# Optimization experiments

Measured on AMD Instinct MI355X. Metric: run time of the kernel, lower is better.

## Reference

```python
import jax, jax.numpy as jnp
import numpy as np

N1, F_IN, E1 = 50000, 128, 1000000   # data1: 10 graphs x 5000 nodes
B, NPG = 10, 5000
N2, E2 = 199, 4000                    # data2: fixed by fc1 in-dim 9950 = 50*199
K = 50
LN_EPS = 1e-5


def setup_inputs() -> dict:
    key = jax.random.key(0)
    ks = jax.random.split(key, 24)
    s = lambda k, shape: (jax.random.normal(k, shape, jnp.float32) * 0.05)
    inp = {}
    inp["x1"] = jax.random.normal(ks[0], (N1, F_IN), jnp.float32)
    inp["edge_index1"] = jax.random.randint(ks[1], (2, E1), 0, N1, jnp.int32)
    inp["batch1"] = jnp.repeat(jnp.arange(B, dtype=jnp.int32), NPG)  # equal-size graphs
    inp["x2"] = jax.random.normal(ks[2], (N2, F_IN), jnp.float32)
    inp["edge_index2"] = jax.random.randint(ks[3], (2, E2), 0, N2, jnp.int32)
    # GNN params (shared Siamese weights). PyG SAGEConv: lin_l (aggr, has bias), lin_r (root, no bias)
    inp["w1l"] = s(ks[4], (128, F_IN)); inp["b1l"] = jnp.zeros((128,), jnp.float32)
    inp["w1r"] = s(ks[5], (128, F_IN))
    inp["w2l"] = s(ks[6], (64, 128));   inp["b2l"] = jnp.zeros((64,), jnp.float32)
    inp["w2r"] = s(ks[7], (64, 128))
    # MLP head
    inp["fc1_w"] = s(ks[8], (128, K * N2)); inp["fc1_b"] = jnp.zeros((128,), jnp.float32)
    inp["ln1_g"] = jnp.ones((128,), jnp.float32); inp["ln1_b"] = jnp.zeros((128,), jnp.float32)
    inp["fc2_w"] = s(ks[9], (64, 128)); inp["fc2_b"] = jnp.zeros((64,), jnp.float32)
    inp["ln2_g"] = jnp.ones((64,), jnp.float32); inp["ln2_b"] = jnp.zeros((64,), jnp.float32)
    inp["fc3_w"] = s(ks[10], (1, 64)); inp["fc3_b"] = jnp.zeros((1,), jnp.float32)
    return inp


def _sage(x, edge_index, wl, bl, wr, n_nodes):
    # mean aggregation of source features at target nodes, then two linears
    src, dst = edge_index[0], edge_index[1]
    msg_sum = jax.ops.segment_sum(x[src], dst, num_segments=n_nodes)
    cnt = jax.ops.segment_sum(jnp.ones((edge_index.shape[1], 1), x.dtype), dst,
                              num_segments=n_nodes)
    mean = msg_sum / jnp.maximum(cnt, 1.0)
    return mean @ wl.T + bl + x @ wr.T


def _gnn(x, ei, w1l, b1l, w1r, w2l, b2l, w2r):
    n = x.shape[0]
    h = jax.nn.relu(_sage(x, ei, w1l, b1l, w1r, n))
    return jax.nn.relu(_sage(h, ei, w2l, b2l, w2r, n))


def _layernorm(x, g, b):
    mu = jnp.mean(x, -1, keepdims=True)
    var = jnp.mean((x - mu) ** 2, -1, keepdims=True)
    return (x - mu) * jax.lax.rsqrt(var + LN_EPS) * g + b


def reference(x1, edge_index1, batch1, x2, edge_index2,
              w1l, b1l, w1r, w2l, b2l, w2r,
              fc1_w, fc1_b, ln1_g, ln1_b, fc2_w, fc2_b, ln2_g, ln2_b, fc3_w, fc3_b):
    out1 = _gnn(x1, edge_index1, w1l, b1l, w1r, w2l, b2l, w2r)   # [N1, 64]
    out2 = _gnn(x2, edge_index2, w1l, b1l, w1r, w2l, b2l, w2r)   # [N2, 64]
    # cdist p=2
    a2 = jnp.sum(out1 * out1, -1, keepdims=True)                 # [N1,1]
    b2 = jnp.sum(out2 * out2, -1)                                # [N2]
    d2 = a2 + b2[None, :] - 2.0 * (out1 @ out2.T)
    dist = jnp.sqrt(jnp.maximum(d2, 0.0))                        # [N1, N2]
    # SortAggregation(k=50): per-graph sort rows by last column (desc), take top k.
    # batch1 groups equal-size graphs contiguously -> reshape is exact dense batching.
    xb = dist.reshape(B, NPG, N2)
    order = jnp.argsort(-xb[:, :, -1], axis=1)[:, :K]            # [B, K]
    topk = jnp.take_along_axis(xb, order[:, :, None], axis=1)    # [B, K, N2]
    out = topk.reshape(B, K * N2)
    out = jax.nn.relu(_layernorm(out @ fc1_w.T + fc1_b, ln1_g, ln1_b))
    out = jax.nn.relu(_layernorm(out @ fc2_w.T + fc2_b, ln2_g, ln2_b))
    out = jax.nn.sigmoid(out @ fc3_w.T + fc3_b)                  # [B, 1]
    return out
```

## Files before the change

### kernel.cpp

```cpp
#include <hip/hip_runtime.h>
#include <math.h>

#define N1 50000
#define F_IN 128
#define E1 1000000
#define Bg 10
#define NPG 5000
#define N2 199
#define E2 4000
#define KSEL 50
#define LN_EPS 1e-5f
#define CHUNKS 16
#define CHSZ 313
#define EBT 4096
#define NB 196
#define BCAP 6144

typedef unsigned long long ull;

__global__ void k_bucket(const int* __restrict__ ei1, int* __restrict__ bcnt,
                         unsigned int* __restrict__ bed,
                         const int* __restrict__ ei2, int* __restrict__ rp2,
                         int* __restrict__ srcs2) {
  int t = threadIdx.x;
  int blk = blockIdx.x;
  const int nEdgeBlocks = (E1 + EBT - 1) / EBT;
  if (blk == nEdgeBlocks) {
    __shared__ int cnt2[N2];
    __shared__ int cur2[N2];
    const int* src = ei2;
    const int* dst = ei2 + E2;
    for (int i = t; i < N2; i += 256) cnt2[i] = 0;
    __syncthreads();
    for (int e = t; e < E2; e += 256) atomicAdd(&cnt2[dst[e]], 1);
    __syncthreads();
    if (t == 0) {
      int run = 0;
      rp2[0] = 0;
      for (int i = 0; i < N2; i++) {
        cur2[i] = run;
        run += cnt2[i];
        rp2[i + 1] = run;
      }
    }
    __syncthreads();
    for (int e = t; e < E2; e += 256) {
      int d = dst[e];
      int pos = atomicAdd(&cur2[d], 1);
      srcs2[pos] = src[e];
    }
    return;
  }
  __shared__ int hcnt[NB];
  const int* src = ei1;
  const int* dst = ei1 + E1;
  int e0 = blk * EBT;
  int e1 = min(e0 + EBT, E1);
  if (t < NB) hcnt[t] = 0;
  __syncthreads();
  for (int e = e0 + t; e < e1; e += 256) atomicAdd(&hcnt[dst[e] >> 8], 1);
  __syncthreads();
  if (t < NB) hcnt[t] = atomicAdd(&bcnt[t], hcnt[t]);
  __syncthreads();
  for (int e = e0 + t; e < e1; e += 256) {
    int d = dst[e];
    int s = src[e];
    int b = d >> 8;
    int pos = atomicAdd(&hcnt[b], 1);
    if (pos < BCAP)
      bed[(size_t)b * BCAP + pos] = ((unsigned int)(d & 255) << 16) | (unsigned int)s;
  }
}

__global__ __launch_bounds__(1024) void k_csr_bucket(
    const int* __restrict__ bcnt, const unsigned int* __restrict__ bed,
    int* __restrict__ rp, int* __restrict__ srcs) {
  __shared__ int cnt[256];
  __shared__ int cur[256];
  __shared__ int wsums[4];
  __shared__ int s_bbase;
  int b = blockIdx.x, t = threadIdx.x;
  int lane = t & 63, w = t >> 6;
  int total = min(bcnt[b], BCAP);
  if (t < 256) cnt[t] = 0;
  if (w == 0) {
    int vb = 0;
    for (int i = lane; i < b; i += 64) vb += min(bcnt[i], BCAP);
    for (int off = 32; off; off >>= 1) vb += __shfl_xor(vb, off);
    if (lane == 0) s_bbase = vb;
  }
  __syncthreads();
  const unsigned int* list = bed + (size_t)b * BCAP;
  for (int e = t; e < total; e += 1024) atomicAdd(&cnt[list[e] >> 16], 1);
  __syncthreads();
  int incl = 0, v = 0;
  if (t < 256) {
    v = cnt[t];
    int x = v;
#pragma unroll
    for (int off = 1; off < 64; off <<= 1) {
      int y = __shfl_up(x, off);
      if (lane >= off) x += y;
    }
    if (lane == 63) wsums[w] = x;
    incl = x;
  }
  __syncthreads();
  if (t < 256) {
    int pre = 0;
    for (int i = 0; i < w; i++) pre += wsums[i];
    incl += pre;
    int bbase = s_bbase;
    int node = b * 256 + t;
    if (node < N1) rp[node + 1] = bbase + incl;
    cur[t] = bbase + incl - v;
    if (b == 0 && t == 0) rp[0] = 0;
  }
  __syncthreads();
  for (int e = t; e < total; e += 1024) {
    unsigned int pe = list[e];
    int pos = atomicAdd(&cur[pe >> 16], 1);
    srcs[pos] = (int)(pe & 0xFFFFu);
  }
}

__global__ void k_aggr128(const float* __restrict__ xA, const int* __restrict__ rpA,
                          const int* __restrict__ srcsA, float* __restrict__ meanA, int nA,
                          const float* __restrict__ xB, const int* __restrict__ rpB,
                          const int* __restrict__ srcsB, float* __restrict__ meanB, int nB,
                          int blocksA) {
  int blk = blockIdx.x;
  const float* x;
  const int* rp;
  const int* srcs;
  float* mean;
  int n, nb0;
  if (blk < blocksA) { x = xA; rp = rpA; srcs = srcsA; mean = meanA; n = nA; nb0 = blk * 4; }
  else { x = xB; rp = rpB; srcs = srcsB; mean = meanB; n = nB; nb0 = (blk - blocksA) * 4; }
  int lane = threadIdx.x & 63;
  int node = nb0 + (threadIdx.x >> 6);
  if (node >= n) return;
  int s = rp[node], e = rp[node + 1];
  int half = lane >> 5;
  int sub = lane & 31;
  const float4* xp = (const float4*)x;
  float4 acc = make_float4(0.f, 0.f, 0.f, 0.f);
  int i = s;
  for (; i + 8 <= e; i += 8) {
    int s0 = srcs[i + half];
    int s1 = srcs[i + 2 + half];
    int s2 = srcs[i + 4 + half];
    int s3 = srcs[i + 6 + half];
    float4 v0 = xp[(size_t)s0 * 32 + sub];
    float4 v1 = xp[(size_t)s1 * 32 + sub];
    float4 v2 = xp[(size_t)s2 * 32 + sub];
    float4 v3 = xp[(size_t)s3 * 32 + sub];
    acc.x += (v0.x + v1.x) + (v2.x + v3.x);
    acc.y += (v0.y + v1.y) + (v2.y + v3.y);
    acc.z += (v0.z + v1.z) + (v2.z + v3.z);
    acc.w += (v0.w + v1.w) + (v2.w + v3.w);
  }
  for (; i + 2 <= e; i += 2) {
    int s0 = srcs[i + half];
    float4 v = xp[(size_t)s0 * 32 + sub];
    acc.x += v.x; acc.y += v.y; acc.z += v.z; acc.w += v.w;
  }
  if (i < e && half == 0) {
    float4 v = xp[(size_t)srcs[i] * 32 + sub];
    acc.x += v.x; acc.y += v.y; acc.z += v.z; acc.w += v.w;
  }
  acc.x += __shfl_xor(acc.x, 32);
  acc.y += __shfl_xor(acc.y, 32);
  acc.z += __shfl_xor(acc.z, 32);
  acc.w += __shfl_xor(acc.w, 32);
  if (half == 0) {
    float c = (float)((e - s) > 0 ? (e - s) : 1);
    float inv = 1.f / c;
    float4 o = make_float4(acc.x * inv, acc.y * inv, acc.z * inv, acc.w * inv);
    ((float4*)mean)[(size_t)node * 32 + sub] = o;
  }
}

__global__ void k_aggr_fused64(const float* __restrict__ zA, const int* __restrict__ rpA,
                               const int* __restrict__ srcsA, float* __restrict__ outA, int nA,
                               const float* __restrict__ zB, const int* __restrict__ rpB,
                               const int* __restrict__ srcsB, float* __restrict__ outB, int nB,
                               const float* __restrict__ bias, int blocksA) {
  int blk = blockIdx.x;
  const float* zlr;
  const int* rp;
  const int* srcs;
  float* out;
  int n, nb0;
  if (blk < blocksA) { zlr = zA; rp = rpA; srcs = srcsA; out = outA; n = nA; nb0 = blk * 4; }
  else { zlr = zB; rp = rpB; srcs = srcsB; out = outB; n = nB; nb0 = (blk - blocksA) * 4; }
  int lane = threadIdx.x & 63;
  int node = nb0 + (threadIdx.x >> 6);
  if (node >= n) return;
  int s = rp[node], e = rp[node + 1];
  int q = lane >> 4;
  int sub = lane & 15;
  const float4* zp = (const float4*)zlr;
  float4 acc = make_float4(0.f, 0.f, 0.f, 0.f);
  int i = s;
  for (; i + 8 <= e; i += 8) {
    int s0 = srcs[i + q];
    int s1 = srcs[i + 4 + q];
    float4 v0 = zp[(size_t)s0 * 32 + sub];
    float4 v1 = zp[(size_t)s1 * 32 + sub];
    acc.x += v0.x + v1.x;
    acc.y += v0.y + v1.y;
    acc.z += v0.z + v1.z;
    acc.w += v0.w + v1.w;
  }
  for (; i + 4 <= e; i += 4) {
    int s0 = srcs[i + q];
    float4 v = zp[(size_t)s0 * 32 + sub];
    acc.x += v.x; acc.y += v.y; acc.z += v.z; acc.w += v.w;
  }
  int rem = e - i;
  if (q < rem) {
    int s0 = srcs[i + q];
    float4 v = zp[(size_t)s0 * 32 + sub];
    acc.x += v.x; acc.y += v.y; acc.z += v.z; acc.w += v.w;
  }
  acc.x += __shfl_xor(acc.x, 16);
  acc.y += __shfl_xor(acc.y, 16);
  acc.z += __shfl_xor(acc.z, 16);
  acc.w += __shfl_xor(acc.w, 16);
  acc.x += __shfl_xor(acc.x, 32);
  acc.y += __shfl_xor(acc.y, 32);
  acc.z += __shfl_xor(acc.z, 32);
  acc.w += __shfl_xor(acc.w, 32);
  if (q == 0) {
    float c = (float)((e - s) > 0 ? (e - s) : 1);
    float inv = 1.f / c;
    float4 mb = ((const float4*)bias)[sub];
    float4 rt = zp[(size_t)node * 32 + 16 + sub];
    float v0 = acc.x * inv + mb.x + rt.x;
    float v1 = acc.y * inv + mb.y + rt.y;
    float v2 = acc.z * inv + mb.z + rt.z;
    float v3 = acc.w * inv + mb.w + rt.w;
    float4 o;
    o.x = v0 > 0.f ? v0 : 0.f;
    o.y = v1 > 0.f ? v1 : 0.f;
    o.z = v2 > 0.f ? v2 : 0.f;
    o.w = v3 > 0.f ? v3 : 0.f;
    ((float4*)out)[(size_t)node * 16 + sub] = o;
  }
}

__global__ __launch_bounds__(256) void k_sage_gemm128(
    const float* __restrict__ xinA, const float* __restrict__ meanA,
    float* __restrict__ outA, int nA,
    const float* __restrict__ xinB, const float* __restrict__ meanB,
    float* __restrict__ outB, int nB,
    const float* __restrict__ wl, const float* __restrict__ bl,
    const float* __restrict__ wr, int blocksA) {
  constexpr int TM = 128, TK = 32;
  constexpr int SA = TM + 4;
  constexpr int SW = 128 + 4;
  __shared__ float s_a[TK][SA];
  __shared__ float s_w[TK][SW];
  int blk = blockIdx.x;
  const float* xin;
  const float* mean;
  float* out;
  int n, m0;
  if (blk < blocksA) { xin = xinA; mean = meanA; out = outA; n = nA; m0 = blk * TM; }
  else { xin = xinB; mean = meanB; out = outB; n = nB; m0 = (blk - blocksA) * TM; }
  int t = threadIdx.x;
  int tx = t & 15, ty = t >> 4;
  int sub = t >> 3;
  int kv = (t & 7) << 2;

  float acc[8][8];
#pragma unroll
  for (int i = 0; i < 8; i++)
#pragma unroll
    for (int j = 0; j < 8; j++) acc[i][j] = 0.f;

  for (int ph = 0; ph < 2; ph++) {
    const float* A = ph ? xin : mean;
    const float* W = ph ? wr : wl;
    for (int k0 = 0; k0 < 128; k0 += TK) {
      __syncthreads();
#pragma unroll
      for (int p = 0; p < 4; p++) {
        int node = m0 + p * 32 + sub;
        float4 v = make_float4(0.f, 0.f, 0.f, 0.f);
        if (node < n) v = *(const float4*)&A[(size_t)node * 128 + k0 + kv];
        int col = p * 32 + sub;
        s_a[kv + 0][col] = v.x;
        s_a[kv + 1][col] = v.y;
        s_a[kv + 2][col] = v.z;
        s_a[kv + 3][col] = v.w;
      }
#pragma unroll
      for (int p = 0; p < 4; p++) {
        int j = p * 32 + sub;
        float4 v = *(const float4*)&W[(size_t)j * 128 + k0 + kv];
        s_w[kv + 0][j] = v.x;
        s_w[kv + 1][j] = v.y;
        s_w[kv + 2][j] = v.z;
        s_w[kv + 3][j] = v.w;
      }
      __syncthreads();
#pragma unroll 8
      for (int kk = 0; kk < TK; kk++) {
        float4 a0 = *(const float4*)&s_a[kk][ty * 8];
        float4 a1 = *(const float4*)&s_a[kk][ty * 8 + 4];
        float av[8] = {a0.x, a0.y, a0.z, a0.w, a1.x, a1.y, a1.z, a1.w};
        float4 w0 = *(const float4*)&s_w[kk][tx * 8];
        float4 w1 = *(const float4*)&s_w[kk][tx * 8 + 4];
        float wv[8] = {w0.x, w0.y, w0.z, w0.w, w1.x, w1.y, w1.z, w1.w};
#pragma unroll
        for (int i = 0; i < 8; i++)
#pragma unroll
          for (int j = 0; j < 8; j++) acc[i][j] = fmaf(av[i], wv[j], acc[i][j]);
      }
    }
  }
  float bj[8];
#pragma unroll
  for (int j = 0; j < 8; j++) bj[j] = bl[tx * 8 + j];
#pragma unroll
  for (int i = 0; i < 8; i++) {
    int node = m0 + ty * 8 + i;
    if (node < n) {
#pragma unroll
      for (int q = 0; q < 8; q += 4) {
        float v0 = acc[i][q + 0] + bj[q + 0];
        float v1 = acc[i][q + 1] + bj[q + 1];
        float v2 = acc[i][q + 2] + bj[q + 2];
        float v3 = acc[i][q + 3] + bj[q + 3];
        float4 o;
        o.x = v0 > 0.f ? v0 : 0.f;
        o.y = v1 > 0.f ? v1 : 0.f;
        o.z = v2 > 0.f ? v2 : 0.f;
        o.w = v3 > 0.f ? v3 : 0.f;
        *(float4*)&out[(size_t)node * 128 + tx * 8 + q] = o;
      }
    }
  }
}

__global__ __launch_bounds__(256) void k_lin_dual(
    const float* __restrict__ AA, float* __restrict__ zA, int nA,
    const float* __restrict__ AB, float* __restrict__ zB, int nB,
    const float* __restrict__ wl, const float* __restrict__ wr, int blocksA) {
  constexpr int TM = 128, TK = 32;
  constexpr int SA = TM + 4;
  constexpr int SW = 128 + 4;
  __shared__ float s_a[TK][SA];
  __shared__ float s_w[TK][SW];
  int blk = blockIdx.x;
  const float* A;
  float* zlr;
  int n, m0;
  if (blk < blocksA) { A = AA; zlr = zA; n = nA; m0 = blk * TM; }
  else { A = AB; zlr = zB; n = nB; m0 = (blk - blocksA) * TM; }
  int t = threadIdx.x;
  int tx = t & 15, ty = t >> 4;
  int sub = t >> 3;
  int kv = (t & 7) << 2;

  float acc[8][8];
#pragma unroll
  for (int i = 0; i < 8; i++)
#pragma unroll
    for (int j = 0; j < 8; j++) acc[i][j] = 0.f;

  for (int k0 = 0; k0 < 128; k0 += TK) {
    __syncthreads();
#pragma unroll
    for (int p = 0; p < 4; p++) {
      int node = m0 + p * 32 + sub;
      float4 v = make_float4(0.f, 0.f, 0.f, 0.f);
      if (node < n) v = *(const float4*)&A[(size_t)node * 128 + k0 + kv];
      int col = p * 32 + sub;
      s_a[kv + 0][col] = v.x;
      s_a[kv + 1][col] = v.y;
      s_a[kv + 2][col] = v.z;
      s_a[kv + 3][col] = v.w;
    }
#pragma unroll
    for (int p = 0; p < 4; p++) {
      int j = p * 32 + sub;
      const float* W = (j < 64) ? &wl[(size_t)j * 128] : &wr[(size_t)(j - 64) * 128];
      float4 v = *(const float4*)&W[k0 + kv];
      s_w[kv + 0][j] = v.x;
      s_w[kv + 1][j] = v.y;
      s_w[kv + 2][j] = v.z;
      s_w[kv + 3][j] = v.w;
    }
    __syncthreads();
#pragma unroll 8
    for (int kk = 0; kk < TK; kk++) {
      float4 a0 = *(const float4*)&s_a[kk][ty * 8];
      float4 a1 = *(const float4*)&s_a[kk][ty * 8 + 4];
      float av[8] = {a0.x, a0.y, a0.z, a0.w, a1.x, a1.y, a1.z, a1.w};
      float4 w0 = *(const float4*)&s_w[kk][tx * 8];
      float4 w1 = *(const float4*)&s_w[kk][tx * 8 + 4];
      float wv[8] = {w0.x, w0.y, w0.z, w0.w, w1.x, w1.y, w1.z, w1.w};
#pragma unroll
      for (int i = 0; i < 8; i++)
#pragma unroll
        for (int j = 0; j < 8; j++) acc[i][j] = fmaf(av[i], wv[j], acc[i][j]);
    }
  }
#pragma unroll
  for (int i = 0; i < 8; i++) {
    int node = m0 + ty * 8 + i;
    if (node < n) {
#pragma unroll
      for (int q = 0; q < 8; q += 4) {
        float4 o = make_float4(acc[i][q + 0], acc[i][q + 1], acc[i][q + 2], acc[i][q + 3]);
        *(float4*)&zlr[(size_t)node * 128 + tx * 8 + q] = o;
      }
    }
  }
}

__global__ void k_score_topk_local(const float* __restrict__ out1,
                                   const float* __restrict__ out2,
                                   ull* __restrict__ cand) {
  __shared__ ull s[512];
  __shared__ float brow[64];
  int blk = blockIdx.x;
  int b = blk >> 4, c = blk & 15;
  int t = threadIdx.x;
  if (t < 64) brow[t] = out2[198 * 64 + t];
  __syncthreads();
  const float4* b4 = (const float4*)brow;
  float b2 = 0.f;
#pragma unroll
  for (int q = 0; q < 16; q++) {
    float4 w = b4[q];
    b2 = fmaf(w.x, w.x, fmaf(w.y, w.y, fmaf(w.z, w.z, fmaf(w.w, w.w, b2))));
  }
#pragma unroll
  for (int p = 0; p < 2; p++) {
    int i = p * 256 + t;
    ull key = 0ULL;
    int gidx = c * CHSZ + i;
    if (i < CHSZ && gidx < NPG) {
      const float4* ap = (const float4*)&out1[((size_t)b * NPG + gidx) * 64];
      float dot = 0.f, a2 = 0.f;
#pragma unroll
      for (int q = 0; q < 16; q++) {
        float4 a = ap[q];
        float4 w = b4[q];
        dot = fmaf(a.x, w.x, fmaf(a.y, w.y, fmaf(a.z, w.z, fmaf(a.w, w.w, dot))));
        a2 = fmaf(a.x, a.x, fmaf(a.y, a.y, fmaf(a.z, a.z, fmaf(a.w, a.w, a2))));
      }
      float d2 = a2 + b2 - 2.f * dot;
      float sc = sqrtf(fmaxf(d2, 0.f));
      key = ((ull)__float_as_uint(sc) << 32) | (unsigned int)(~gidx);
    }
    s[i] = key;
  }
  __syncthreads();
  for (int k = 2; k <= 512; k <<= 1) {
    for (int j = k >> 1; j > 0; j >>= 1) {
#pragma unroll
      for (int p = 0; p < 2; p++) {
        int i = p * 256 + t;
        int l = i ^ j;
        if (l > i) {
          bool up = ((i & k) != 0);
          ull a = s[i], bb = s[l];
          if ((a > bb) == up) { s[i] = bb; s[l] = a; }
        }
      }
      __syncthreads();
    }
  }
  if (t < KSEL) cand[(b * CHUNKS + c) * KSEL + t] = s[t];
}

__global__ void k_topk_merge(const ull* __restrict__ cand, int* __restrict__ sel) {
  __shared__ ull s[1024];
  int b = blockIdx.x, t = threadIdx.x;
#pragma unroll
  for (int p = 0; p < 4; p++) {
    int i = p * 256 + t;
    s[i] = (i < CHUNKS * KSEL) ? cand[b * CHUNKS * KSEL + i] : 0ULL;
  }
  __syncthreads();
  for (int k = 2; k <= 1024; k <<= 1) {
    for (int j = k >> 1; j > 0; j >>= 1) {
#pragma unroll
      for (int p = 0; p < 4; p++) {
        int i = p * 256 + t;
        int l = i ^ j;
        if (l > i) {
          bool up = ((i & k) != 0);
          ull a = s[i], bb = s[l];
          if ((a > bb) == up) { s[i] = bb; s[l] = a; }
        }
      }
      __syncthreads();
    }
  }
  if (t < KSEL) {
    int gidx = (int)(~((unsigned int)s[t]));
    sel[b * KSEL + t] = b * NPG + gidx;
  }
}

__global__ void k_dist_rows(const float* __restrict__ out1, const float* __restrict__ out2,
                            const int* __restrict__ sel, float* __restrict__ D) {
  __shared__ float arow[64];
  int i = blockIdx.x;
  int t = threadIdx.x;
  int node = sel[i];
  if (t < 64) arow[t] = out1[(size_t)node * 64 + t];
  __syncthreads();
  float a2 = 0.f;
#pragma unroll
  for (int f = 0; f < 64; f++) a2 = fmaf(arow[f], arow[f], a2);
  for (int nn = t; nn < N2; nn += 256) {
    float dot = 0.f, b2 = 0.f;
#pragma unroll 8
    for (int f = 0; f < 64; f++) {
      float bv = out2[nn * 64 + f];
      dot = fmaf(arow[f], bv, dot);
      b2 = fmaf(bv, bv, b2);
    }
    float d2 = a2 + b2 - 2.f * dot;
    D[i * N2 + nn] = sqrtf(fmaxf(d2, 0.f));
  }
}

__global__ void k_fc1_dot(const float* __restrict__ D, const float* __restrict__ w,
                          float* __restrict__ h1pre) {
  constexpr int M = KSEL * N2;
  constexpr int M2 = M / 2;
  int j = blockIdx.x;
  int t = threadIdx.x;
  const float2* wp = (const float2*)(w + (size_t)j * M);
  float acc[Bg];
#pragma unroll
  for (int b = 0; b < Bg; b++) acc[b] = 0.f;
  for (int m = t; m < M2; m += 256) {
    float2 wv = wp[m];
#pragma unroll
    for (int b = 0; b < Bg; b++) {
      float2 dv = ((const float2*)(D + (size_t)b * M))[m];
      acc[b] = fmaf(dv.x, wv.x, fmaf(dv.y, wv.y, acc[b]));
    }
  }
  __shared__ float ws_[4][Bg];
  int lane = t & 63, wv_ = t >> 6;
#pragma unroll
  for (int b = 0; b < Bg; b++) {
    float v = acc[b];
    for (int off = 32; off; off >>= 1) v += __shfl_xor(v, off);
    if (lane == 0) ws_[wv_][b] = v;
  }
  __syncthreads();
  if (t < Bg) h1pre[t * 128 + j] = ws_[0][t] + ws_[1][t] + ws_[2][t] + ws_[3][t];
}

__global__ void k_fc123(const float* __restrict__ h1pre, const float* __restrict__ fc1b,
                        const float* __restrict__ g1, const float* __restrict__ be1,
                        const float* __restrict__ w2, const float* __restrict__ b2v,
                        const float* __restrict__ g2, const float* __restrict__ be2,
                        const float* __restrict__ w3, const float* __restrict__ b3,
                        float* __restrict__ out) {
  __shared__ float wsum[2];
  __shared__ float sh[128];
  int b = blockIdx.x, t = threadIdx.x;
  float acc = h1pre[b * 128 + t] + fc1b[t];
  int lane = t & 63, wv_ = t >> 6;
  float ssum = acc;
  for (int off = 32; off; off >>= 1) ssum += __shfl_xor(ssum, off);
  if (lane == 0) wsum[wv_] = ssum;
  __syncthreads();
  float mu = (wsum[0] + wsum[1]) / 128.f;
  __syncthreads();
  float d = acc - mu;
  float vv = d * d;
  for (int off = 32; off; off >>= 1) vv += __shfl_xor(vv, off);
  if (lane == 0) wsum[wv_] = vv;
  __syncthreads();
  float var = (wsum[0] + wsum[1]) / 128.f;
  float r = rsqrtf(var + LN_EPS);
  float h = d * r * g1[t] + be1[t];
  sh[t] = h > 0.f ? h : 0.f;
  __syncthreads();
  if (t < 64) {
    float a2 = b2v[t];
#pragma unroll 8
    for (int k = 0; k < 128; k++) a2 = fmaf(sh[k], w2[t * 128 + k], a2);
    float s2 = a2;
    for (int off = 32; off; off >>= 1) s2 += __shfl_xor(s2, off);
    float mu2 = s2 * (1.f / 64.f);
    float d2 = a2 - mu2;
    float vv2 = d2 * d2;
    for (int off = 32; off; off >>= 1) vv2 += __shfl_xor(vv2, off);
    float r2 = rsqrtf(vv2 * (1.f / 64.f) + LN_EPS);
    float h2 = d2 * r2 * g2[t] + be2[t];
    h2 = h2 > 0.f ? h2 : 0.f;
    float pp = h2 * w3[t];
    for (int off = 32; off; off >>= 1) pp += __shfl_xor(pp, off);
    if (t == 0) out[b] = 1.f / (1.f + expf(-(pp + b3[0])));
  }
}

extern "C" void kernel_launch(void* const* d_in, const int* in_sizes, int n_in,
                              void* d_out, int out_size, void* d_ws, size_t ws_size,
                              hipStream_t stream) {
  const float* x1 = (const float*)d_in[0];
  const int* ei1 = (const int*)d_in[1];
  const float* x2 = (const float*)d_in[3];
  const int* ei2 = (const int*)d_in[4];
  const float* w1l = (const float*)d_in[5];
  const float* b1l = (const float*)d_in[6];
  const float* w1r = (const float*)d_in[7];
  const float* w2l = (const float*)d_in[8];
  const float* b2l = (const float*)d_in[9];
  const float* w2r = (const float*)d_in[10];
  const float* fc1w = (const float*)d_in[11];
  const float* fc1b = (const float*)d_in[12];
  const float* ln1g = (const float*)d_in[13];
  const float* ln1b = (const float*)d_in[14];
  const float* fc2w = (const float*)d_in[15];
  const float* fc2b = (const float*)d_in[16];
  const float* ln2g = (const float*)d_in[17];
  const float* ln2b = (const float*)d_in[18];
  const float* fc3w = (const float*)d_in[19];
  const float* fc3b = (const float*)d_in[20];
  float* out = (float*)d_out;

  char* p = (char*)d_ws;
  auto alloc = [&](size_t bytes) {
    char* r = p;
    p += (bytes + 255) & ~(size_t)255;
    return r;
  };
  int* rp1 = (int*)alloc((N1 + 1) * 4);
  int* bcnt = (int*)alloc(NB * 4);
  unsigned int* bed = (unsigned int*)alloc((size_t)NB * BCAP * 4);
  int* srcs1 = (int*)alloc((size_t)E1 * 4);
  int* rp2 = (int*)alloc((N2 + 1) * 4);
  int* srcs2 = (int*)alloc(E2 * 4);
  float* bufMean = (float*)alloc((size_t)N1 * 128 * 4);
  float* bufH = (float*)alloc((size_t)N1 * 128 * 4);
  float* out1b = (float*)alloc((size_t)N1 * 64 * 4);
  float* mean2 = (float*)alloc((size_t)N2 * 128 * 4);
  float* h2g = (float*)alloc((size_t)N2 * 128 * 4);
  float* out2b = (float*)alloc((size_t)N2 * 64 * 4);
  int* sel = (int*)alloc(Bg * KSEL * 4);
  ull* cand = (ull*)alloc((size_t)Bg * CHUNKS * KSEL * 8);
  float* Dm = (float*)alloc((size_t)Bg * KSEL * N2 * 4);
  float* h1pre = (float*)alloc(Bg * 128 * 4);

  const int nEdgeBlocks = (E1 + EBT - 1) / EBT;
  const int aggrBlocksA = (N1 + 3) / 4;
  const int aggrBlocksB = (N2 + 3) / 4;
  const int gemmBlocksA = (N1 + 127) / 128;
  const int gemmBlocksB = (N2 + 127) / 128;

  hipMemsetAsync(bcnt, 0, NB * 4, stream);
  k_bucket<<<nEdgeBlocks + 1, 256, 0, stream>>>(ei1, bcnt, bed, ei2, rp2, srcs2);
  k_csr_bucket<<<NB, 1024, 0, stream>>>(bcnt, bed, rp1, srcs1);
  k_aggr128<<<aggrBlocksA + aggrBlocksB, 256, 0, stream>>>(
      x1, rp1, srcs1, bufMean, N1, x2, rp2, srcs2, mean2, N2, aggrBlocksA);
  k_sage_gemm128<<<gemmBlocksA + gemmBlocksB, 256, 0, stream>>>(
      x1, bufMean, bufH, N1, x2, mean2, h2g, N2, w1l, b1l, w1r, gemmBlocksA);
  k_lin_dual<<<gemmBlocksA + gemmBlocksB, 256, 0, stream>>>(
      bufH, bufMean, N1, h2g, mean2, N2, w2l, w2r, gemmBlocksA);
  k_aggr_fused64<<<aggrBlocksA + aggrBlocksB, 256, 0, stream>>>(
      bufMean, rp1, srcs1, out1b, N1, mean2, rp2, srcs2, out2b, N2, b2l, aggrBlocksA);
  k_score_topk_local<<<Bg * CHUNKS, 256, 0, stream>>>(out1b, out2b, cand);
  k_topk_merge<<<Bg, 256, 0, stream>>>(cand, sel);
  k_dist_rows<<<Bg * KSEL, 256, 0, stream>>>(out1b, out2b, sel, Dm);
  k_fc1_dot<<<128, 256, 0, stream>>>(Dm, fc1w, h1pre);
  k_fc123<<<Bg, 128, 0, stream>>>(h1pre, fc1b, ln1g, ln1b, fc2w, fc2b, ln2g, ln2b,
                                  fc3w, fc3b, out);
}
```

Before: 391.2 us.

## Slice feature columns across blocks in neighbor aggregation kernels

Both mean-aggregation kernels now split the feature dimension into slices, one slice per block, with 8 slices for the 128-wide pass and 4 for the 64-wide pass. Within a slice, 16 edges are processed in parallel per wavefront with 4 lanes per edge. The aim is to improve L2 locality, since blocks at the same time touch only a narrow column slab of the source features, and to expose more parallelism for short adjacency lists. In exchange, srcs and rp are reread once per slice, each gather is only 64 bytes per row, more shuffle reductions are needed, and the manual unrolling is gone.

```diff
diff --git a/kernel.cpp b/kernel.cpp
--- a/kernel.cpp
+++ b/kernel.cpp
@@ -124,119 +124,97 @@
   }
 }
 
-__global__ void k_aggr128(const float* __restrict__ xA, const int* __restrict__ rpA,
-                          const int* __restrict__ srcsA, float* __restrict__ meanA, int nA,
-                          const float* __restrict__ xB, const int* __restrict__ rpB,
-                          const int* __restrict__ srcsB, float* __restrict__ meanB, int nB,
-                          int blocksA) {
+__global__ void k_aggr128_sliced(const float* __restrict__ xA, const int* __restrict__ rpA,
+                                 const int* __restrict__ srcsA, float* __restrict__ meanA,
+                                 int nA,
+                                 const float* __restrict__ xB, const int* __restrict__ rpB,
+                                 const int* __restrict__ srcsB, float* __restrict__ meanB,
+                                 int nB, int groupsA) {
   int blk = blockIdx.x;
+  int slice = blk & 7;
+  int grp = blk >> 3;
   const float* x;
   const int* rp;
   const int* srcs;
   float* mean;
-  int n, nb0;
-  if (blk < blocksA) { x = xA; rp = rpA; srcs = srcsA; mean = meanA; n = nA; nb0 = blk * 4; }
-  else { x = xB; rp = rpB; srcs = srcsB; mean = meanB; n = nB; nb0 = (blk - blocksA) * 4; }
+  int n, node0;
+  if (grp < groupsA) { x = xA; rp = rpA; srcs = srcsA; mean = meanA; n = nA; node0 = grp * 4; }
+  else { x = xB; rp = rpB; srcs = srcsB; mean = meanB; n = nB; node0 = (grp - groupsA) * 4; }
   int lane = threadIdx.x & 63;
-  int node = nb0 + (threadIdx.x >> 6);
+  int node = node0 + (threadIdx.x >> 6);
   if (node >= n) return;
   int s = rp[node], e = rp[node + 1];
-  int half = lane >> 5;
-  int sub = lane & 31;
+  int slot = lane >> 2;
+  int sub = lane & 3;
   const float4* xp = (const float4*)x;
   float4 acc = make_float4(0.f, 0.f, 0.f, 0.f);
-  int i = s;
-  for (; i + 8 <= e; i += 8) {
-    int s0 = srcs[i + half];
-    int s1 = srcs[i + 2 + half];
-    int s2 = srcs[i + 4 + half];
-    int s3 = srcs[i + 6 + half];
-    float4 v0 = xp[(size_t)s0 * 32 + sub];
-    float4 v1 = xp[(size_t)s1 * 32 + sub];
-    float4 v2 = xp[(size_t)s2 * 32 + sub];
-    float4 v3 = xp[(size_t)s3 * 32 + sub];
-    acc.x += (v0.x + v1.x) + (v2.x + v3.x);
-    acc.y += (v0.y + v1.y) + (v2.y + v3.y);
-    acc.z += (v0.z + v1.z) + (v2.z + v3.z);
-    acc.w += (v0.w + v1.w) + (v2.w + v3.w);
-  }
-  for (; i + 2 <= e; i += 2) {
-    int s0 = srcs[i + half];
-    float4 v = xp[(size_t)s0 * 32 + sub];
-    acc.x += v.x; acc.y += v.y; acc.z += v.z; acc.w += v.w;
-  }
-  if (i < e && half == 0) {
-    float4 v = xp[(size_t)srcs[i] * 32 + sub];
-    acc.x += v.x; acc.y += v.y; acc.z += v.z; acc.w += v.w;
-  }
-  acc.x += __shfl_xor(acc.x, 32);
-  acc.y += __shfl_xor(acc.y, 32);
-  acc.z += __shfl_xor(acc.z, 32);
-  acc.w += __shfl_xor(acc.w, 32);
-  if (half == 0) {
+  for (int i = s; i < e; i += 16) {
+    int ei = i + slot;
+    if (ei < e) {
+      int sv = srcs[ei];
+      float4 v = xp[(size_t)sv * 32 + slice * 4 + sub];
+      acc.x += v.x; acc.y += v.y; acc.z += v.z; acc.w += v.w;
+    }
+  }
+#pragma unroll
+  for (int off = 4; off < 64; off <<= 1) {
+    acc.x += __shfl_xor(acc.x, off);
+    acc.y += __shfl_xor(acc.y, off);
+    acc.z += __shfl_xor(acc.z, off);
+    acc.w += __shfl_xor(acc.w, off);
+  }
+  if (slot == 0) {
     float c = (float)((e - s) > 0 ? (e - s) : 1);
     float inv = 1.f / c;
     float4 o = make_float4(acc.x * inv, acc.y * inv, acc.z * inv, acc.w * inv);
-    ((float4*)mean)[(size_t)node * 32 + sub] = o;
-  }
-}
-
-__global__ void k_aggr_fused64(const float* __restrict__ zA, const int* __restrict__ rpA,
-                               const int* __restrict__ srcsA, float* __restrict__ outA, int nA,
-                               const float* __restrict__ zB, const int* __restrict__ rpB,
-                               const int* __restrict__ srcsB, float* __restrict__ outB, int nB,
-                               const float* __restrict__ bias, int blocksA) {
+    ((float4*)mean)[(size_t)node * 32 + slice * 4 + sub] = o;
+  }
+}
+
+__global__ void k_aggr_fused64_sliced(const float* __restrict__ zA, const int* __restrict__ rpA,
+                                      const int* __restrict__ srcsA, float* __restrict__ outA,
+                                      int nA,
+                                      const float* __restrict__ zB, const int* __restrict__ rpB,
+                                      const int* __restrict__ srcsB, float* __restrict__ outB,
+                                      int nB, const float* __restrict__ bias, int groupsA) {
   int blk = blockIdx.x;
+  int slice = blk & 3;
+  int grp = blk >> 2;
   const float* zlr;
   const int* rp;
   const int* srcs;
   float* out;
-  int n, nb0;
-  if (blk < blocksA) { zlr = zA; rp = rpA; srcs = srcsA; out = outA; n = nA; nb0 = blk * 4; }
-  else { zlr = zB; rp = rpB; srcs = srcsB; out = outB; n = nB; nb0 = (blk - blocksA) * 4; }
+  int n, node0;
+  if (grp < groupsA) { zlr = zA; rp = rpA; srcs = srcsA; out = outA; n = nA; node0 = grp * 4; }
+  else { zlr = zB; rp = rpB; srcs = srcsB; out = outB; n = nB; node0 = (grp - groupsA) * 4; }
   int lane = threadIdx.x & 63;
-  int node = nb0 + (threadIdx.x >> 6);
+  int node = node0 + (threadIdx.x >> 6);
   if (node >= n) return;
   int s = rp[node], e = rp[node + 1];
-  int q = lane >> 4;
-  int sub = lane & 15;
+  int slot = lane >> 2;
+  int sub = lane & 3;
   const float4* zp = (const float4*)zlr;
   float4 acc = make_float4(0.f, 0.f, 0.f, 0.f);
-  int i = s;
-  for (; i + 8 <= e; i += 8) {
-    int s0 = srcs[i + q];
-    int s1 = srcs[i + 4 + q];
-    float4 v0 = zp[(size_t)s0 * 32 + sub];
-    float4 v1 = zp[(size_t)s1 * 32 + sub];
-    acc.x += v0.x + v1.x;
-    acc.y += v0.y + v1.y;
-    acc.z += v0.z + v1.z;
-    acc.w += v0.w + v1.w;
-  }
-  for (; i + 4 <= e; i += 4) {
-    int s0 = srcs[i + q];
-    float4 v = zp[(size_t)s0 * 32 + sub];
-    acc.x += v.x; acc.y += v.y; acc.z += v.z; acc.w += v.w;
-  }
-  int rem = e - i;
-  if (q < rem) {
-    int s0 = srcs[i + q];
-    float4 v = zp[(size_t)s0 * 32 + sub];
-    acc.x += v.x; acc.y += v.y; acc.z += v.z; acc.w += v.w;
-  }
-  acc.x += __shfl_xor(acc.x, 16);
-  acc.y += __shfl_xor(acc.y, 16);
-  acc.z += __shfl_xor(acc.z, 16);
-  acc.w += __shfl_xor(acc.w, 16);
-  acc.x += __shfl_xor(acc.x, 32);
-  acc.y += __shfl_xor(acc.y, 32);
-  acc.z += __shfl_xor(acc.z, 32);
-  acc.w += __shfl_xor(acc.w, 32);
-  if (q == 0) {
+  for (int i = s; i < e; i += 16) {
+    int ei = i + slot;
+    if (ei < e) {
+      int sv = srcs[ei];
+      float4 v = zp[(size_t)sv * 32 + slice * 4 + sub];
+      acc.x += v.x; acc.y += v.y; acc.z += v.z; acc.w += v.w;
+    }
+  }
+#pragma unroll
+  for (int off = 4; off < 64; off <<= 1) {
+    acc.x += __shfl_xor(acc.x, off);
+    acc.y += __shfl_xor(acc.y, off);
+    acc.z += __shfl_xor(acc.z, off);
+    acc.w += __shfl_xor(acc.w, off);
+  }
+  if (slot == 0) {
     float c = (float)((e - s) > 0 ? (e - s) : 1);
     float inv = 1.f / c;
-    float4 mb = ((const float4*)bias)[sub];
-    float4 rt = zp[(size_t)node * 32 + 16 + sub];
+    float4 mb = ((const float4*)bias)[slice * 4 + sub];
+    float4 rt = zp[(size_t)node * 32 + 16 + slice * 4 + sub];
     float v0 = acc.x * inv + mb.x + rt.x;
     float v1 = acc.y * inv + mb.y + rt.y;
     float v2 = acc.z * inv + mb.z + rt.z;
@@ -246,7 +224,7 @@
     o.y = v1 > 0.f ? v1 : 0.f;
     o.z = v2 > 0.f ? v2 : 0.f;
     o.w = v3 > 0.f ? v3 : 0.f;
-    ((float4*)out)[(size_t)node * 16 + sub] = o;
+    ((float4*)out)[(size_t)node * 16 + slice * 4 + sub] = o;
   }
 }
 
@@ -658,22 +636,22 @@
   float* h1pre = (float*)alloc(Bg * 128 * 4);
 
   const int nEdgeBlocks = (E1 + EBT - 1) / EBT;
-  const int aggrBlocksA = (N1 + 3) / 4;
-  const int aggrBlocksB = (N2 + 3) / 4;
+  const int groupsA = (N1 + 3) / 4;
+  const int groupsB = (N2 + 3) / 4;
   const int gemmBlocksA = (N1 + 127) / 128;
   const int gemmBlocksB = (N2 + 127) / 128;
 
   hipMemsetAsync(bcnt, 0, NB * 4, stream);
   k_bucket<<<nEdgeBlocks + 1, 256, 0, stream>>>(ei1, bcnt, bed, ei2, rp2, srcs2);
   k_csr_bucket<<<NB, 1024, 0, stream>>>(bcnt, bed, rp1, srcs1);
-  k_aggr128<<<aggrBlocksA + aggrBlocksB, 256, 0, stream>>>(
-      x1, rp1, srcs1, bufMean, N1, x2, rp2, srcs2, mean2, N2, aggrBlocksA);
+  k_aggr128_sliced<<<(groupsA + groupsB) * 8, 256, 0, stream>>>(
+      x1, rp1, srcs1, bufMean, N1, x2, rp2, srcs2, mean2, N2, groupsA);
   k_sage_gemm128<<<gemmBlocksA + gemmBlocksB, 256, 0, stream>>>(
       x1, bufMean, bufH, N1, x2, mean2, h2g, N2, w1l, b1l, w1r, gemmBlocksA);
   k_lin_dual<<<gemmBlocksA + gemmBlocksB, 256, 0, stream>>>(
       bufH, bufMean, N1, h2g, mean2, N2, w2l, w2r, gemmBlocksA);
-  k_aggr_fused64<<<aggrBlocksA + aggrBlocksB, 256, 0, stream>>>(
-      bufMean, rp1, srcs1, out1b, N1, mean2, rp2, srcs2, out2b, N2, b2l, aggrBlocksA);
+  k_aggr_fused64_sliced<<<(groupsA + groupsB) * 4, 256, 0, stream>>>(
+      bufMean, rp1, srcs1, out1b, N1, mean2, rp2, srcs2, out2b, N2, b2l, groupsA);
   k_score_topk_local<<<Bg * CHUNKS, 256, 0, stream>>>(out1b, out2b, cand);
   k_topk_merge<<<Bg, 256, 0, stream>>>(cand, sel);
   k_dist_rows<<<Bg * KSEL, 256, 0, stream>>>(out1b, out2b, sel, Dm);
```

Measured after the change: 486.5 us. 24.4% more time.
